# Performance work log

Hardware: AMD Instinct MI355X
Metric: run time of the kernel (lower is better)

## Reference

```python
import jax, jax.numpy as jnp
import numpy as np
from jax import lax


def setup_inputs() -> dict:
    key = jax.random.key(0)
    ks = jax.random.split(key, 12)
    B, L, C = 256, 1024, 16
    F = C * ((L + 10 * L) // 2)  # 90112
    inp = {
        "x": jax.random.normal(ks[0], (B, L), jnp.float32),
        "leaf_w": jax.random.normal(ks[1], (L, C), jnp.float32) * 0.05,
        "leaf_b": jax.random.normal(ks[2], (L, C), jnp.float32) * 0.05,
        "conv_w": jax.random.normal(ks[3], (C, C, 3), jnp.float32) * 0.05,
        "conv_b": jax.random.normal(ks[4], (C,), jnp.float32) * 0.05,
        "bn_gamma": jnp.ones((C,), jnp.float32),
        "bn_beta": jnp.zeros((C,), jnp.float32),
        "node_weights": jax.random.uniform(ks[5], (2 * L - 1,), jnp.float32),
        "fc1_w": jax.random.normal(ks[6], (128, F), jnp.float32) * 0.01,
        "fc1_b": jax.random.normal(ks[7], (128,), jnp.float32) * 0.01,
        "fc2_w": jax.random.normal(ks[8], (64, 128), jnp.float32) * 0.05,
        "fc2_b": jax.random.normal(ks[9], (64,), jnp.float32) * 0.05,
        "fc3_w": jax.random.normal(ks[10], (1, 64), jnp.float32) * 0.05,
        "fc3_b": jax.random.normal(ks[11], (1,), jnp.float32) * 0.05,
    }
    return inp


def reference(x, leaf_w, leaf_b, conv_w, conv_b, bn_gamma, bn_beta,
              node_weights, fc1_w, fc1_b, fc2_w, fc2_b, fc3_w, fc3_b):
    B, L = x.shape
    C = leaf_w.shape[1]
    D = int(np.log2(L))  # perfect binary tree depth
    EPS = 1e-5

    # per-leaf 1x1 conv (distinct weights per leaf) + per-leaf node weight
    leaf = x[:, :, None] * leaf_w[None] + leaf_b[None]           # [B,L,C]
    leaf = leaf * node_weights[:L][None, :, None]
    all_feats = [jnp.transpose(leaf, (0, 2, 1))]                  # [B,C,L] (leaf length 1 each)

    bn_scale = bn_gamma / jnp.sqrt(1.0 + EPS)                     # eval-mode BN (mean=0, var=1)

    X = leaf[:, :, :, None]                                       # [B,N,C,len]
    offset = L
    for _ in range(D):
        Bn, N, Cc, Lk = X.shape
        N2 = N // 2
        # concat sibling pairs along length
        Y = X.reshape(Bn, N2, 2, Cc, Lk).transpose(0, 1, 3, 2, 4).reshape(Bn, N2, Cc, 2 * Lk)
        Z = Y.reshape(Bn * N2, Cc, 2 * Lk)
        Z = lax.conv_general_dilated(Z, conv_w, window_strides=(1,), padding="SAME",
                                     dimension_numbers=("NCH", "OIH", "NCH"))
        Z = Z + conv_b[None, :, None]
        Z = Z * bn_scale[None, :, None] + bn_beta[None, :, None]
        Z = jax.nn.relu(Z)
        Z = Z.reshape(Bn, N2, Cc, 2 * Lk)
        Z = Z * node_weights[offset:offset + N2][None, :, None, None]
        offset += N2
        all_feats.append(Z.transpose(0, 2, 1, 3).reshape(Bn, Cc, N2 * 2 * Lk))
        X = Z

    comb = jnp.concatenate(all_feats, axis=2)                     # [B,C,T]
    T = comb.shape[2]
    pooled = comb[:, :, : (T // 2) * 2].reshape(B, C, T // 2, 2).max(-1)  # MaxPool1d(2)
    flat = pooled.reshape(B, -1)
    h = jax.nn.relu(flat @ fc1_w.T + fc1_b)
    h = jax.nn.relu(h @ fc2_w.T + fc2_b)
    return h @ fc3_w.T + fc3_b
```

## Files before the change

### kernel.cpp

```cpp
#include <hip/hip_runtime.h>
#include <hip/hip_bf16.h>

#define BATCH 256
#define L 1024
#define C 16
#define POOL 512
#define PCOLS 5632
#define FDIM 90112
#define H1 128
#define H2 64

#define KS 256
#define KCHUNK (FDIM / KS)

#define SROW 24
#define SBUF (1025 * SROW)
#define TREE_LDS_BYTES (2 * SBUF * 2)

#define TROW 520

typedef float f32x4 __attribute__((ext_vector_type(4)));
typedef short bf16x8 __attribute__((ext_vector_type(8)));
typedef unsigned long long u64;

__device__ __forceinline__ unsigned short f2b(float f) {
    union { __hip_bfloat16 h; unsigned short u; } cv;
    cv.h = __float2bfloat16(f);
    return cv.u;
}
__device__ __forceinline__ unsigned int pk(float lo, float hi) {
    return (unsigned int)f2b(lo) | ((unsigned int)f2b(hi) << 16);
}

__launch_bounds__(1024, 4)
__global__ void tree_kernel(const float* __restrict__ x,
                            const float* __restrict__ leaf_w,
                            const float* __restrict__ leaf_b,
                            const float* __restrict__ conv_w,
                            const float* __restrict__ conv_b,
                            const float* __restrict__ bn_gamma,
                            const float* __restrict__ bn_beta,
                            const float* __restrict__ node_w,
                            unsigned short* __restrict__ pooledb,
                            const float* __restrict__ w1,
                            unsigned short* __restrict__ w1p) {
    extern __shared__ short smem[];
    short* buf0 = smem;
    short* buf1 = smem + SBUF;

    const int b   = blockIdx.x;
    const int tid = threadIdx.x;
    const int lane = tid & 63;
    const int wv   = tid >> 6;
    const int n    = lane & 15;
    const int g    = lane >> 4;

    if (tid < SROW) {
        buf0[1024 * SROW + tid] = 0;
        buf1[1024 * SROW + tid] = 0;
    }

    bf16x8 A1, A2;
#pragma unroll
    for (int j = 0; j < 8; ++j) {
        const int ci = (g & 1) * 8 + j;
        A1[j] = (short)f2b(conv_w[(n * C + ci) * 3 + (g >> 1)]);
        A2[j] = (g < 2) ? (short)f2b(conv_w[(n * C + ci) * 3 + 2]) : (short)0;
    }
    float sc4[4], bt4[4];
#pragma unroll
    for (int r = 0; r < 4; ++r) {
        const int co = g * 4 + r;
        float s = bn_gamma[co] / sqrtf(1.0f + 1e-5f);
        sc4[r] = s;
        bt4[r] = conv_b[co] * s + bn_beta[co];
    }

    {
        const float xv = x[b * L + tid];
        const float nw = node_w[tid];
        const float4* lwa = (const float4*)(leaf_w + 16 * tid);
        const float4* lba = (const float4*)(leaf_b + 16 * tid);
        short* row = buf0 + tid * SROW;
#pragma unroll 1
        for (int q = 0; q < 4; ++q) {
            float4 wq = lwa[q], bq = lba[q];
            float v0 = (xv * wq.x + bq.x) * nw;
            float v1 = (xv * wq.y + bq.y) * nw;
            float v2 = (xv * wq.z + bq.z) * nw;
            float v3 = (xv * wq.w + bq.w) * nw;
            *(u64*)(row + 4 * q) =
                (u64)pk(v0, v1) | ((u64)pk(v2, v3) << 32);
            float p0 = fmaxf(v0, __shfl_xor(v0, 1));
            float p1 = fmaxf(v1, __shfl_xor(v1, 1));
            float p2 = fmaxf(v2, __shfl_xor(v2, 1));
            float p3 = fmaxf(v3, __shfl_xor(v3, 1));
            if (!(tid & 1)) {
                *(u64*)(pooledb + (long)b * FDIM + (tid >> 1) * 16 + 4 * q) =
                    (u64)pk(p0, p1) | ((u64)pk(p2, p3) << 32);
            }
        }
        __syncthreads();
    }

    short* bin  = buf0;
    short* bout = buf1;
    int noff = L;
    for (int d = 0; d < 10; ++d) {
        const int sh = d + 1;
        const int mask = (1 << sh) - 1;

        bf16x8 B1s[4], B2s[4];
#pragma unroll
        for (int ti = 0; ti < 4; ++ti) {
            const int pos = (wv * 4 + ti) * 16 + n;
            const bool ok1 = (g >= 2) || ((pos & mask) != 0);
            const int r1 = ok1 ? (pos + (g >> 1) - 1) : 1024;
            B1s[ti] = *(const bf16x8*)(bin + r1 * SROW + (g & 1) * 8);
            const bool ok2 = ((pos & mask) != mask);
            const int r2 = ok2 ? (pos + 1) : 1024;
            B2s[ti] = *(const bf16x8*)(bin + r2 * SROW + (g & 1) * 8);
        }

#pragma unroll
        for (int ti = 0; ti < 4; ++ti) {
            const int pos = (wv * 4 + ti) * 16 + n;

            f32x4 acc = {0.f, 0.f, 0.f, 0.f};
            acc = __builtin_amdgcn_mfma_f32_16x16x32_bf16(A1, B1s[ti], acc, 0, 0, 0);
            acc = __builtin_amdgcn_mfma_f32_16x16x32_bf16(A2, B2s[ti], acc, 0, 0, 0);

            const float nwv = node_w[noff + (pos >> sh)];
            float z[4];
#pragma unroll
            for (int r = 0; r < 4; ++r)
                z[r] = fmaxf(fmaf(sc4[r], acc[r], bt4[r]), 0.f) * nwv;

            if (d < 9) {
                *(u64*)(bout + pos * SROW + g * 4) =
                    (u64)pk(z[0], z[1]) | ((u64)pk(z[2], z[3]) << 32);
            }

            float pz0 = fmaxf(z[0], __shfl_xor(z[0], 1));
            float pz1 = fmaxf(z[1], __shfl_xor(z[1], 1));
            float pz2 = fmaxf(z[2], __shfl_xor(z[2], 1));
            float pz3 = fmaxf(z[3], __shfl_xor(z[3], 1));
            if (!(n & 1)) {
                *(u64*)(pooledb + (long)b * FDIM + sh * 8192 + (pos >> 1) * 16 + g * 4) =
                    (u64)pk(pz0, pz1) | ((u64)pk(pz2, pz3) << 32);
            }
        }

        if (d >= 5 && d < 9) {
            __syncthreads();
        } else {
            asm volatile("s_waitcnt lgkmcnt(0)" ::: "memory");
        }

        short* t = bin; bin = bout; bout = t;
        noff += (512 >> d);
    }

    __syncthreads();

    unsigned short* st = (unsigned short*)smem;
    for (int unit = b; unit < 11 * H1; unit += BATCH) {
        const int lev = unit >> 7;
        const int nr  = unit & 127;
        const float* src = w1 + (long)nr * FDIM + lev * POOL;
#pragma unroll 2
        for (int i = tid; i < 2048; i += 1024) {
            const int c = i >> 7, q = i & 127;
            float4 v = *(const float4*)(src + (long)c * PCOLS + 4 * q);
            *(u64*)(st + c * TROW + 4 * q) =
                (u64)pk(v.x, v.y) | ((u64)pk(v.z, v.w) << 32);
        }
        __syncthreads();
#pragma unroll 2
        for (int i = tid; i < 2048; i += 1024) {
            const int pos2 = i >> 2, c4 = i & 3;
            unsigned short s0 = st[(c4 * 4 + 0) * TROW + pos2];
            unsigned short s1 = st[(c4 * 4 + 1) * TROW + pos2];
            unsigned short s2 = st[(c4 * 4 + 2) * TROW + pos2];
            unsigned short s3 = st[(c4 * 4 + 3) * TROW + pos2];
            *(u64*)(w1p + (long)nr * FDIM + lev * 8192 + pos2 * 16 + c4 * 4) =
                (u64)s0 | ((u64)s1 << 16) | ((u64)s2 << 32) | ((u64)s3 << 48);
        }
        __syncthreads();
    }
}

__launch_bounds__(512, 2)
__global__ void fc1_mfma(const unsigned short* __restrict__ pooledb,
                         const unsigned short* __restrict__ w1b,
                         float* __restrict__ partial) {
    const int ks  = blockIdx.x;

    const int tid  = threadIdx.x;
    const int wv   = tid >> 6;
    const int lane = tid & 63;
    const int lrow = lane & 15;
    const int lk   = (lane >> 4) * 8;

    const int m0 = wv * 32;
    const int kb = ks * KCHUNK;

    const unsigned short* ap0 = pooledb + (long)(m0 + lrow) * FDIM + kb + lk;
    const unsigned short* ap1 = ap0 + (long)16 * FDIM;
    const unsigned short* bp  = w1b + (long)lrow * FDIM + kb + lk;

    f32x4 acc[2][8];
#pragma unroll
    for (int i = 0; i < 2; ++i)
#pragma unroll
        for (int ct = 0; ct < 8; ++ct) acc[i][ct] = (f32x4){0.f, 0.f, 0.f, 0.f};

#pragma unroll 1
    for (int kk = 0; kk < KCHUNK; kk += 32) {
        bf16x8 a0 = *(const bf16x8*)(ap0 + kk);
        bf16x8 a1 = *(const bf16x8*)(ap1 + kk);
#pragma unroll
        for (int ct = 0; ct < 8; ++ct) {
            bf16x8 bv = *(const bf16x8*)(bp + (long)(ct * 16) * FDIM + kk);
            acc[0][ct] = __builtin_amdgcn_mfma_f32_16x16x32_bf16(a0, bv, acc[0][ct], 0, 0, 0);
            acc[1][ct] = __builtin_amdgcn_mfma_f32_16x16x32_bf16(a1, bv, acc[1][ct], 0, 0, 0);
        }
    }

    const int rbase = (lane >> 4) * 4;
#pragma unroll
    for (int i = 0; i < 2; ++i) {
#pragma unroll
        for (int r = 0; r < 4; ++r) {
            const int row = m0 + i * 16 + rbase + r;
            float* p = partial + (long)row * (KS * H1) + ks * H1 + (lane & 15);
#pragma unroll
            for (int ct = 0; ct < 8; ++ct)
                p[ct * 16] = acc[i][ct][r];
        }
    }
}

__launch_bounds__(1024)
__global__ void fc_tail(const float* __restrict__ partial,
                        const float* __restrict__ fc1_b,
                        const float* __restrict__ w2,
                        const float* __restrict__ b2,
                        const float* __restrict__ w3,
                        const float* __restrict__ b3,
                        float* __restrict__ out, int nkt) {
    __shared__ float red[8][H1];
    __shared__ float h1_s[H1];
    __shared__ float w2_s[H2 * 129];

    const int b = blockIdx.x;
    const int tid = threadIdx.x;
    const int t = tid & 127;
    const int q = tid >> 7;

    const int per = nkt >> 3;
    float s = 0.f;
    const float* pb = partial + (long)b * (KS * H1) + (q * per) * H1 + t;
#pragma unroll 8
    for (int kt = 0; kt < per; ++kt)
        s += pb[kt * H1];
    red[q][t] = s;

    for (int i = tid; i < H2 * H1; i += 1024) {
        int j = i >> 7, k = i & 127;
        w2_s[j * 129 + k] = w2[i];
    }
    __syncthreads();

    if (tid < 128) {
        float ss = red[0][t] + red[1][t] + red[2][t] + red[3][t]
                 + red[4][t] + red[5][t] + red[6][t] + red[7][t];
        h1_s[t] = fmaxf(ss + fc1_b[t], 0.f);
    }
    __syncthreads();

    if (tid < 64) {
        float a2 = 0.f;
#pragma unroll 8
        for (int k = 0; k < H1; ++k) a2 = fmaf(h1_s[k], w2_s[tid * 129 + k], a2);
        float h2 = fmaxf(a2 + b2[tid], 0.f);
        float r = h2 * w3[tid];
#pragma unroll
        for (int off = 32; off > 0; off >>= 1) r += __shfl_down(r, off);
        if (tid == 0) out[b] = r + b3[0];
    }
}

extern "C" void kernel_launch(void* const* d_in, const int* in_sizes, int n_in,
                              void* d_out, int out_size, void* d_ws, size_t ws_size,
                              hipStream_t stream) {
    const float* x        = (const float*)d_in[0];
    const float* leaf_w   = (const float*)d_in[1];
    const float* leaf_b   = (const float*)d_in[2];
    const float* conv_w   = (const float*)d_in[3];
    const float* conv_b   = (const float*)d_in[4];
    const float* bn_gamma = (const float*)d_in[5];
    const float* bn_beta  = (const float*)d_in[6];
    const float* node_w   = (const float*)d_in[7];
    const float* fc1_w    = (const float*)d_in[8];
    const float* fc1_b    = (const float*)d_in[9];
    const float* fc2_w    = (const float*)d_in[10];
    const float* fc2_b    = (const float*)d_in[11];
    const float* fc3_w    = (const float*)d_in[12];
    const float* fc3_b    = (const float*)d_in[13];

    unsigned short* pooledb = (unsigned short*)d_ws;
    unsigned short* w1p     = pooledb + (long)BATCH * FDIM;
    float*          partial = (float*)(w1p + (long)H1 * FDIM);

    (void)hipFuncSetAttribute((const void*)tree_kernel,
                        hipFuncAttributeMaxDynamicSharedMemorySize, TREE_LDS_BYTES);

    tree_kernel<<<BATCH, 1024, TREE_LDS_BYTES, stream>>>(
        x, leaf_w, leaf_b, conv_w, conv_b, bn_gamma, bn_beta, node_w, pooledb,
        fc1_w, w1p);

    fc1_mfma<<<KS, 512, 0, stream>>>(pooledb, w1p, partial);

    fc_tail<<<BATCH, 1024, 0, stream>>>(partial, fc1_b, fc2_w, fc2_b, fc3_w, fc3_b,
                                        (float*)d_out, KS);
}
```

Baseline: 89.04 us.

## Interleave fc1 weight repacking into tree levels and cache node weights in LDS

```diff
diff --git a/kernel.cpp b/kernel.cpp
--- a/kernel.cpp
+++ b/kernel.cpp
@@ -15,9 +15,7 @@
 
 #define SROW 24
 #define SBUF (1025 * SROW)
-#define TREE_LDS_BYTES (2 * SBUF * 2)
-
-#define TROW 520
+#define TREE_LDS_BYTES (2 * SBUF * 2 + 2047 * 4)
 
 typedef float f32x4 __attribute__((ext_vector_type(4)));
 typedef short bf16x8 __attribute__((ext_vector_type(8)));
@@ -47,6 +45,7 @@
     extern __shared__ short smem[];
     short* buf0 = smem;
     short* buf1 = smem + SBUF;
+    float* nwl  = (float*)(smem + 2 * SBUF);
 
     const int b   = blockIdx.x;
     const int tid = threadIdx.x;
@@ -59,6 +58,7 @@
         buf0[1024 * SROW + tid] = 0;
         buf1[1024 * SROW + tid] = 0;
     }
+    for (int i = tid; i < 2047; i += 1024) nwl[i] = node_w[i];
 
     bf16x8 A1, A2;
 #pragma unroll
@@ -75,6 +75,8 @@
         sc4[r] = s;
         bt4[r] = conv_b[co] * s + bn_beta[co];
     }
+
+    const int gbase = b * 11264 + tid;
 
     {
         const float xv = x[b * L + tid];
@@ -110,6 +112,22 @@
         const int sh = d + 1;
         const int mask = (1 << sh) - 1;
 
+        {
+            const int gidx = gbase + d * 1024;
+            const int pos2 = gidx & 511;
+            const int c4   = (gidx >> 9) & 3;
+            const int un   = gidx >> 11;
+            const int lev  = un >> 7;
+            const int nr   = un & 127;
+            const float* src = w1 + (long)nr * FDIM + lev * POOL + pos2;
+            float f0 = src[(c4 * 4 + 0) * PCOLS];
+            float f1 = src[(c4 * 4 + 1) * PCOLS];
+            float f2 = src[(c4 * 4 + 2) * PCOLS];
+            float f3 = src[(c4 * 4 + 3) * PCOLS];
+            *(u64*)(w1p + (long)nr * FDIM + lev * 8192 + pos2 * 16 + c4 * 4) =
+                (u64)pk(f0, f1) | ((u64)pk(f2, f3) << 32);
+        }
+
         bf16x8 B1s[4], B2s[4];
 #pragma unroll
         for (int ti = 0; ti < 4; ++ti) {
@@ -130,7 +148,7 @@
             acc = __builtin_amdgcn_mfma_f32_16x16x32_bf16(A1, B1s[ti], acc, 0, 0, 0);
             acc = __builtin_amdgcn_mfma_f32_16x16x32_bf16(A2, B2s[ti], acc, 0, 0, 0);
 
-            const float nwv = node_w[noff + (pos >> sh)];
+            const float nwv = nwl[noff + (pos >> sh)];
             float z[4];
 #pragma unroll
             for (int r = 0; r < 4; ++r)
@@ -161,32 +179,20 @@
         noff += (512 >> d);
     }
 
-    __syncthreads();
-
-    unsigned short* st = (unsigned short*)smem;
-    for (int unit = b; unit < 11 * H1; unit += BATCH) {
-        const int lev = unit >> 7;
-        const int nr  = unit & 127;
-        const float* src = w1 + (long)nr * FDIM + lev * POOL;
-#pragma unroll 2
-        for (int i = tid; i < 2048; i += 1024) {
-            const int c = i >> 7, q = i & 127;
-            float4 v = *(const float4*)(src + (long)c * PCOLS + 4 * q);
-            *(u64*)(st + c * TROW + 4 * q) =
-                (u64)pk(v.x, v.y) | ((u64)pk(v.z, v.w) << 32);
-        }
-        __syncthreads();
-#pragma unroll 2
-        for (int i = tid; i < 2048; i += 1024) {
-            const int pos2 = i >> 2, c4 = i & 3;
-            unsigned short s0 = st[(c4 * 4 + 0) * TROW + pos2];
-            unsigned short s1 = st[(c4 * 4 + 1) * TROW + pos2];
-            unsigned short s2 = st[(c4 * 4 + 2) * TROW + pos2];
-            unsigned short s3 = st[(c4 * 4 + 3) * TROW + pos2];
-            *(u64*)(w1p + (long)nr * FDIM + lev * 8192 + pos2 * 16 + c4 * 4) =
-                (u64)s0 | ((u64)s1 << 16) | ((u64)s2 << 32) | ((u64)s3 << 48);
-        }
-        __syncthreads();
+    {
+        const int gidx = gbase + 10 * 1024;
+        const int pos2 = gidx & 511;
+        const int c4   = (gidx >> 9) & 3;
+        const int un   = gidx >> 11;
+        const int lev  = un >> 7;
+        const int nr   = un & 127;
+        const float* src = w1 + (long)nr * FDIM + lev * POOL + pos2;
+        float f0 = src[(c4 * 4 + 0) * PCOLS];
+        float f1 = src[(c4 * 4 + 1) * PCOLS];
+        float f2 = src[(c4 * 4 + 2) * PCOLS];
+        float f3 = src[(c4 * 4 + 3) * PCOLS];
+        *(u64*)(w1p + (long)nr * FDIM + lev * 8192 + pos2 * 16 + c4 * 4) =
+            (u64)pk(f0, f1) | ((u64)pk(f2, f3) << 32);
     }
 }
 
```

Result: faster. 82.21 us (-7.7%).
